# Performance work log

Measured on AMD Instinct MI355X. Metric: run time of the kernel, lower is better.

## Reference

```python
import jax, jax.numpy as jnp
import numpy as np

N = 50000      # nodes
E = 800000     # edges (avg degree 16)
IN = 256       # input feature dim
HID = 128      # hidden dim
H = 4          # heads
C = HID // H   # per-head dim = 32
L = 3          # layers


def setup_inputs() -> dict:
    key = jax.random.key(0)
    ks = jax.random.split(key, 16)
    s = 0.02
    f32 = jnp.float32
    inp = {
        "x": jax.random.normal(ks[0], (N, IN), f32),
        "edge_index": jax.random.randint(ks[1], (2, E), 0, N, dtype=jnp.int32),
        "edge_attr": jax.random.normal(ks[2], (E, 1), f32),
        "Wi": jax.random.normal(ks[3], (IN, HID), f32) * s,
        "bi": jnp.zeros((HID,), f32),
        "Wq": jax.random.normal(ks[4], (L, HID, HID), f32) * s,
        "bq": jnp.zeros((L, HID), f32),
        "Wk": jax.random.normal(ks[5], (L, HID, HID), f32) * s,
        "bk": jnp.zeros((L, HID), f32),
        "Wv": jax.random.normal(ks[6], (L, HID, HID), f32) * s,
        "bv": jnp.zeros((L, HID), f32),
        "We": jax.random.normal(ks[7], (L, 1, HID), f32) * s,      # lin_edge, no bias
        "Wskip": jax.random.normal(ks[8], (L, HID, HID), f32) * s,
        "bskip": jnp.zeros((L, HID), f32),
        "Wbeta": jax.random.normal(ks[9], (L, 3 * HID, 1), f32) * s,  # lin_beta, no bias
        "ln_g": jnp.ones((L, HID), f32),
        "ln_b": jnp.zeros((L, HID), f32),
    }
    return inp


def _layer_norm(x, g, b, eps=1e-5):
    mu = jnp.mean(x, axis=-1, keepdims=True)
    var = jnp.var(x, axis=-1, keepdims=True)
    return (x - mu) * jax.lax.rsqrt(var + eps) * g + b


def _transformer_conv(h, src, dst, edge_attr, Wq, bq, Wk, bk, Wv, bv, We, Wskip, bskip, Wbeta):
    # node-level projections [N, HID]
    q = h @ Wq + bq
    k = h @ Wk + bk
    v = h @ Wv + bv
    e = edge_attr @ We                       # [E, HID] edge embedding
    # per-edge gathered features [E, H, C]
    qi = q[dst].reshape(E, H, C)
    kj = (k[src] + e).reshape(E, H, C)
    vj = (v[src] + e).reshape(E, H, C)
    # attention logits [E, H]
    alpha = jnp.sum(qi * kj, axis=-1) / np.sqrt(C)
    # segment softmax over destination node
    amax = jax.ops.segment_max(alpha, dst, num_segments=N)   # [N, H]
    ex = jnp.exp(alpha - amax[dst])
    denom = jax.ops.segment_sum(ex, dst, num_segments=N)     # [N, H]
    attn = ex / (denom[dst] + 1e-16)                         # [E, H]
    # scatter-add aggregation -> [N, H, C] -> concat heads [N, HID]
    out = jax.ops.segment_sum(attn[..., None] * vj, dst, num_segments=N).reshape(N, HID)
    # gated skip (beta=True, root_weight=True)
    x_r = h @ Wskip + bskip
    beta = jax.nn.sigmoid(jnp.concatenate([out, x_r, out - x_r], axis=-1) @ Wbeta)  # [N, 1]
    return beta * x_r + (1.0 - beta) * out


def reference(x, edge_index, edge_attr, Wi, bi, Wq, bq, Wk, bk, Wv, bv, We, Wskip, bskip, Wbeta, ln_g, ln_b):
    src = edge_index[0]
    dst = edge_index[1]
    h = x @ Wi + bi
    for l in range(L):
        res = h
        h = _transformer_conv(h, src, dst, edge_attr,
                              Wq[l], bq[l], Wk[l], bk[l], Wv[l], bv[l],
                              We[l], Wskip[l], bskip[l], Wbeta[l])
        h = jax.nn.gelu(h, approximate=False)
        h = _layer_norm(h + res, ln_g[l], ln_b[l])
        # dropout: eval mode -> identity
    return h
```

## Files before the change

### kernel.cpp

```cpp
#include <hip/hip_runtime.h>
#include <math.h>

#define NNODES 50000
#define NEDGES 800000
#define DIN 256
#define DHID 128
#define GBLK 391

typedef __attribute__((ext_vector_type(8))) short short8;
typedef __attribute__((ext_vector_type(4))) float f32x4;
typedef __attribute__((ext_vector_type(2))) float f32x2;

__device__ __forceinline__ unsigned short f2bf(float f) {
    unsigned u = __builtin_bit_cast(unsigned, f);
    u += 0x7fffu + ((u >> 16) & 1u);
    return (unsigned short)(u >> 16);
}
__device__ __forceinline__ float bf2f(unsigned short s) {
    return __builtin_bit_cast(float, (unsigned)s << 16);
}
__device__ __forceinline__ unsigned packbf(float a, float b) {
    return (unsigned)f2bf(a) | ((unsigned)f2bf(b) << 16);
}
__device__ __forceinline__ float dpp_xor1(float x) {
    return __builtin_bit_cast(float, __builtin_amdgcn_update_dpp(0, __builtin_bit_cast(int, x), 0xB1, 0xF, 0xF, true));
}
__device__ __forceinline__ float dpp_xor2(float x) {
    return __builtin_bit_cast(float, __builtin_amdgcn_update_dpp(0, __builtin_bit_cast(int, x), 0x4E, 0xF, 0xF, true));
}
__device__ __forceinline__ float dpp_hmirror(float x) {
    return __builtin_bit_cast(float, __builtin_amdgcn_update_dpp(0, __builtin_bit_cast(int, x), 0x141, 0xF, 0xF, true));
}
__device__ __forceinline__ float dpp_mirror(float x) {
    return __builtin_bit_cast(float, __builtin_amdgcn_update_dpp(0, __builtin_bit_cast(int, x), 0x140, 0xF, 0xF, true));
}
__device__ __forceinline__ float red16(float x) {
    x += dpp_xor1(x);
    x += dpp_xor2(x);
    x += dpp_hmirror(x);
    x += dpp_mirror(x);
    return x;
}

__global__ __launch_bounds__(256) void prep_hist(const float* __restrict__ Wi, const float* __restrict__ Wq,
                                                 const float* __restrict__ Wk, const float* __restrict__ Wv,
                                                 const float* __restrict__ Ws, unsigned short* __restrict__ Wit,
                                                 unsigned short* __restrict__ Wt3, const int* __restrict__ dst,
                                                 int* __restrict__ counts, int pb) {
    if ((int)blockIdx.x < pb) {
        int idx = blockIdx.x * 256 + threadIdx.x;
        if (idx < DHID * DIN) {
            int n = idx >> 8, kk = idx & 255;
            Wit[idx] = f2bf(Wi[kk * DHID + n]);
        }
        int idx2 = idx - DHID * DIN;
        if (idx2 >= 0 && idx2 < 3 * 512 * DHID) {
            int l = idx2 / (512 * DHID);
            int rem = idx2 - l * 512 * DHID;
            int r = rem >> 7;
            int kk = rem & 127;
            int sel = r >> 7, rl = r & 127;
            const float* srcm = sel == 0 ? Wq : sel == 1 ? Wk : sel == 2 ? Wv : Ws;
            Wt3[idx2] = f2bf(srcm[l * DHID * DHID + kk * DHID + rl]);
        }
    } else {
        int e = (blockIdx.x - pb) * 256 + threadIdx.x;
        if (e < NEDGES) atomicAdd(&counts[dst[e]], 1);
    }
}

__global__ __launch_bounds__(256) void k_scan_block(const int* __restrict__ in, int* __restrict__ out,
                                                    int* __restrict__ partials, int n) {
    __shared__ int sh[256];
    int tid = threadIdx.x;
    int i = blockIdx.x * 256 + tid;
    int vv = (i < n) ? in[i] : 0;
    sh[tid] = vv;
    __syncthreads();
    for (int off = 1; off < 256; off <<= 1) {
        int t = (tid >= off) ? sh[tid - off] : 0;
        __syncthreads();
        sh[tid] += t;
        __syncthreads();
    }
    if (i < n) out[i] = sh[tid];
    if (tid == 255) partials[blockIdx.x] = sh[255];
}

__global__ __launch_bounds__(256) void k_apply2(const int* __restrict__ partials, int* __restrict__ row_ptr, int n,
                                                int nb) {
    __shared__ int sh[256];
    int tid = threadIdx.x;
    int vv = (tid < nb) ? partials[tid] : 0;
    sh[tid] = vv;
    __syncthreads();
    for (int off = 1; off < 256; off <<= 1) {
        int t = (tid >= off) ? sh[tid - off] : 0;
        __syncthreads();
        sh[tid] += t;
        __syncthreads();
    }
    int i = blockIdx.x * 256 + tid;
    if (i < n) {
        int add = blockIdx.x ? sh[blockIdx.x - 1] : 0;
        row_ptr[i + 1] += add;
    }
    if (i == 0) row_ptr[0] = 0;
}

__global__ __launch_bounds__(256) void scatter_gemm(const float* __restrict__ A, const unsigned short* __restrict__ Wt,
                                                    const float* __restrict__ bias, unsigned* __restrict__ h32, int M,
                                                    const int* __restrict__ src, const int* __restrict__ dst,
                                                    const float* __restrict__ ea, const int* __restrict__ row_ptr,
                                                    int* __restrict__ fill, unsigned* __restrict__ esrc) {
    __shared__ short As[128 * 128];
    const int tid = threadIdx.x;
    if ((int)blockIdx.x >= GBLK) {
        int e = (blockIdx.x - GBLK) * 256 + tid;
        if (e < NEDGES) {
            int d = dst[e];
            int old = atomicSub(&fill[d], 1);
            int pos = row_ptr[d] + old - 1;
            unsigned pk = (unsigned)src[e] | ((unsigned)f2bf(ea[e]) << 16);
            __builtin_nontemporal_store(pk, &esrc[pos]);
        }
        return;
    }
    const int lane = tid & 63;
    const int wid = tid >> 6;
    const int row0 = blockIdx.x * 128;
    const int wr = (wid & 1) * 64;
    const int wc = (wid >> 1) * 64;
    f32x4 acc[4][4] = {};
    const int srow = tid >> 1;
    const int sk = (tid & 1) * 64;
    const int grow = min(row0 + srow, M - 1);
    for (int kt = 0; kt < 2; ++kt) {
        const float* ap = A + (size_t)grow * DIN + kt * 128 + sk;
#pragma unroll
        for (int i = 0; i < 8; ++i) {
            float4 f0 = *(const float4*)(ap + i * 8);
            float4 f1 = *(const float4*)(ap + i * 8 + 4);
            short8 s;
            s[0] = f2bf(f0.x); s[1] = f2bf(f0.y); s[2] = f2bf(f0.z); s[3] = f2bf(f0.w);
            s[4] = f2bf(f1.x); s[5] = f2bf(f1.y); s[6] = f2bf(f1.z); s[7] = f2bf(f1.w);
            int g = (sk >> 3) + i;
            *(short8*)(&As[srow * 128 + ((g ^ (srow & 7)) << 3)]) = s;
        }
        __syncthreads();
#pragma unroll
        for (int ks = 0; ks < 4; ++ks) {
            short8 a[4], b[4];
#pragma unroll
            for (int m = 0; m < 4; ++m) {
                int r = wr + m * 16 + (lane & 15);
                int g = ks * 4 + (lane >> 4);
                a[m] = *(const short8*)(&As[r * 128 + ((g ^ (r & 7)) << 3)]);
            }
#pragma unroll
            for (int n = 0; n < 4; ++n) {
                int c = wc + n * 16 + (lane & 15);
                b[n] = *(const short8*)(Wt + (size_t)c * DIN + kt * 128 + ks * 32 + (lane >> 4) * 8);
            }
#pragma unroll
            for (int m = 0; m < 4; ++m)
#pragma unroll
                for (int n = 0; n < 4; ++n)
                    acc[m][n] = __builtin_amdgcn_mfma_f32_16x16x32_bf16(a[m], b[n], acc[m][n], 0, 0, 0);
        }
        __syncthreads();
    }
    float* my = ((float*)As) + wid * 1024;
    float bb[4];
#pragma unroll
    for (int n = 0; n < 4; ++n) bb[n] = bias[wc + n * 16 + (lane & 15)];
    const int rr = lane >> 2;
    const int cb = lane & 3;
#pragma unroll
    for (int m = 0; m < 4; ++m) {
#pragma unroll
        for (int n = 0; n < 4; ++n) {
            int lc = n * 16 + (lane & 15);
#pragma unroll
            for (int j = 0; j < 4; ++j) {
                int row = (lane >> 4) * 4 + j;
                my[row * 64 + (((lc >> 2) ^ (row & 7)) << 2) + (lc & 3)] = acc[m][n][j] + bb[n];
            }
        }
        float vals[16];
#pragma unroll
        for (int s = 0; s < 4; ++s) {
            int gx = (cb * 4 + s) ^ (rr & 7);
            f32x4 t4 = *(const f32x4*)(my + rr * 64 + gx * 4);
            vals[s * 4 + 0] = t4.x; vals[s * 4 + 1] = t4.y; vals[s * 4 + 2] = t4.z; vals[s * 4 + 3] = t4.w;
        }
        int grow2 = row0 + wr + m * 16 + rr;
        if (grow2 < M) {
            unsigned pk[8];
#pragma unroll
            for (int d = 0; d < 8; ++d) pk[d] = packbf(vals[2 * d], vals[2 * d + 1]);
            unsigned* op = h32 + (size_t)grow2 * 64 + (wc >> 1) + cb * 8;
            *(uint4*)op = make_uint4(pk[0], pk[1], pk[2], pk[3]);
            *(uint4*)(op + 4) = make_uint4(pk[4], pk[5], pk[6], pk[7]);
        }
    }
}

__global__ __launch_bounds__(512) void gemm_qkvs(const unsigned short* __restrict__ A,
                                                 const unsigned short* __restrict__ Wt, const float* __restrict__ bq,
                                                 const float* __restrict__ bk, const float* __restrict__ bv,
                                                 const float* __restrict__ bs, unsigned* __restrict__ q32,
                                                 unsigned* __restrict__ kv, unsigned* __restrict__ xr32, int M) {
    __shared__ short As[128 * 128];
    const int tid = threadIdx.x;
    const int lane = tid & 63;
    const int wid = tid >> 6;
    const int row0 = blockIdx.x * 128;
    const int sel = wid >> 2;
    const int wr = (wid & 1) * 64;
    const int wc = ((wid >> 1) & 1) * 64;
    f32x4 acc0[4][4] = {}, acc1[4][4] = {};
    {
        const int srow = tid >> 2;
        const int sk = (tid & 3) * 32;
        const int grow = min(row0 + srow, M - 1);
        const unsigned short* ap = A + (size_t)grow * DHID + sk;
#pragma unroll
        for (int i = 0; i < 4; ++i) {
            short8 s = *(const short8*)(ap + i * 8);
            int g = (sk >> 3) + i;
            *(short8*)(&As[srow * 128 + ((g ^ (srow & 7)) << 3)]) = s;
        }
    }
    __syncthreads();
    const int b0base = sel ? 128 : 0;
    const int b1base = sel ? 256 : 384;
#pragma unroll
    for (int ks = 0; ks < 4; ++ks) {
        short8 a[4], b0[4], b1[4];
#pragma unroll
        for (int m = 0; m < 4; ++m) {
            int r = wr + m * 16 + (lane & 15);
            int g = ks * 4 + (lane >> 4);
            a[m] = *(const short8*)(&As[r * 128 + ((g ^ (r & 7)) << 3)]);
        }
#pragma unroll
        for (int n = 0; n < 4; ++n) {
            int rb = wc + n * 16 + (lane & 15);
            b0[n] = *(const short8*)(Wt + (size_t)(b0base + rb) * DHID + ks * 32 + (lane >> 4) * 8);
            b1[n] = *(const short8*)(Wt + (size_t)(b1base + rb) * DHID + ks * 32 + (lane >> 4) * 8);
        }
#pragma unroll
        for (int m = 0; m < 4; ++m)
#pragma unroll
            for (int n = 0; n < 4; ++n) {
                acc0[m][n] = __builtin_amdgcn_mfma_f32_16x16x32_bf16(a[m], b0[n], acc0[m][n], 0, 0, 0);
                acc1[m][n] = __builtin_amdgcn_mfma_f32_16x16x32_bf16(a[m], b1[n], acc1[m][n], 0, 0, 0);
            }
    }
    __syncthreads();
    float* my = ((float*)As) + wid * 1024;
    const float* bias0 = sel ? bk : bq;
    const float* bias1 = sel ? bv : bs;
    float bb0[4], bb1[4];
#pragma unroll
    for (int n = 0; n < 4; ++n) {
        int c = wc + n * 16 + (lane & 15);
        bb0[n] = bias0[c];
        bb1[n] = bias1[c];
    }
    const int rr = lane >> 2;
    const int cb = lane & 3;
#pragma unroll
    for (int m = 0; m < 4; ++m) {
        float vals0[16], vals1[16];
#pragma unroll
        for (int n = 0; n < 4; ++n) {
            int lc = n * 16 + (lane & 15);
#pragma unroll
            for (int j = 0; j < 4; ++j) {
                int row = (lane >> 4) * 4 + j;
                my[row * 64 + (((lc >> 2) ^ (row & 7)) << 2) + (lc & 3)] = acc0[m][n][j] + bb0[n];
            }
        }
#pragma unroll
        for (int s = 0; s < 4; ++s) {
            int gx = (cb * 4 + s) ^ (rr & 7);
            f32x4 t4 = *(const f32x4*)(my + rr * 64 + gx * 4);
            vals0[s * 4 + 0] = t4.x; vals0[s * 4 + 1] = t4.y; vals0[s * 4 + 2] = t4.z; vals0[s * 4 + 3] = t4.w;
        }
#pragma unroll
        for (int n = 0; n < 4; ++n) {
            int lc = n * 16 + (lane & 15);
#pragma unroll
            for (int j = 0; j < 4; ++j) {
                int row = (lane >> 4) * 4 + j;
                my[row * 64 + (((lc >> 2) ^ (row & 7)) << 2) + (lc & 3)] = acc1[m][n][j] + bb1[n];
            }
        }
#pragma unroll
        for (int s = 0; s < 4; ++s) {
            int gx = (cb * 4 + s) ^ (rr & 7);
            f32x4 t4 = *(const f32x4*)(my + rr * 64 + gx * 4);
            vals1[s * 4 + 0] = t4.x; vals1[s * 4 + 1] = t4.y; vals1[s * 4 + 2] = t4.z; vals1[s * 4 + 3] = t4.w;
        }
        int grow2 = row0 + wr + m * 16 + rr;
        if (grow2 < M) {
            size_t obase = (size_t)grow2 * 64 + (wc >> 1) + cb * 8;
            if (sel == 0) {
                unsigned p0[8], p1[8];
#pragma unroll
                for (int d = 0; d < 8; ++d) {
                    p0[d] = packbf(vals0[2 * d], vals0[2 * d + 1]);
                    p1[d] = packbf(vals1[2 * d], vals1[2 * d + 1]);
                }
                *(uint4*)(q32 + obase) = make_uint4(p0[0], p0[1], p0[2], p0[3]);
                *(uint4*)(q32 + obase + 4) = make_uint4(p0[4], p0[5], p0[6], p0[7]);
                *(uint4*)(xr32 + obase) = make_uint4(p1[0], p1[1], p1[2], p1[3]);
                *(uint4*)(xr32 + obase + 4) = make_uint4(p1[4], p1[5], p1[6], p1[7]);
            } else {
                unsigned pk[8];
#pragma unroll
                for (int d = 0; d < 8; ++d) {
                    unsigned u = (unsigned)__builtin_amdgcn_cvt_pk_fp8_f32(vals0[2 * d], vals0[2 * d + 1], 0, false);
                    u = (unsigned)__builtin_amdgcn_cvt_pk_fp8_f32(vals1[2 * d], vals1[2 * d + 1], (int)u, true);
                    pk[d] = u;
                }
                *(uint4*)(kv + obase) = make_uint4(pk[0], pk[1], pk[2], pk[3]);
                *(uint4*)(kv + obase + 4) = make_uint4(pk[4], pk[5], pk[6], pk[7]);
            }
        }
    }
}

__global__ __launch_bounds__(256) void node_attn_fuse(const unsigned* __restrict__ q32,
                                                      const unsigned* __restrict__ kv, const unsigned* __restrict__ esrc,
                                                      const float* __restrict__ We, const int* __restrict__ row_ptr,
                                                      const unsigned* __restrict__ xr32, const unsigned* res32,
                                                      const float* __restrict__ Wb, const float* __restrict__ lng,
                                                      const float* __restrict__ lnb, unsigned* houtb, float* houtf) {
    const int tid = threadIdx.x;
    const int lane = tid & 63;
    const int lnl = lane & 15;
    const int gbase = lane & 48;
    const int node = blockIdx.x * 16 + (tid >> 4);
    const int base = row_ptr[node], end = row_ptr[node + 1];
    const float SC = 0.25505654047688565f;
    const float THR = 8.0f;

    float qv[8], wev[8];
    {
        uint4 qw = *(const uint4*)(q32 + (size_t)node * 64 + 4 * lnl);
        unsigned qd[4] = {qw.x, qw.y, qw.z, qw.w};
#pragma unroll
        for (int t = 0; t < 4; ++t) {
            qv[2 * t] = bf2f((unsigned short)qd[t]) * SC;
            qv[2 * t + 1] = bf2f((unsigned short)(qd[t] >> 16)) * SC;
        }
        float4 wlo = *(const float4*)(We + 8 * lnl);
        float4 whi = *(const float4*)(We + 8 * lnl + 4);
        wev[0] = wlo.x; wev[1] = wlo.y; wev[2] = wlo.z; wev[3] = wlo.w;
        wev[4] = whi.x; wev[5] = whi.y; wev[6] = whi.z; wev[7] = whi.w;
    }
    float qwe;
    {
        float s = 0.f;
#pragma unroll
        for (int i = 0; i < 8; ++i) s = fmaf(qv[i], wev[i], s);
        s += dpp_xor1(s);
        s += dpp_xor2(s);
        qwe = s;
    }

    float m = -1e30f, sden = 0.f, tacc = 0.f;
    float acc[8] = {};
    const unsigned* kvp = kv + 4 * lnl;

    for (int off = 0; ; off += 16) {
        int cnt = min(end - base - off, 16);
        if (__all(cnt <= 0)) break;
        unsigned u_l = 0;
        if (lnl < cnt) u_l = esrc[base + off + lnl];
        int cm = max(cnt, 0);
        cm = max(cm, __shfl_xor(cm, 16));
        cm = max(cm, __shfl_xor(cm, 32));
        unsigned ue_n = __shfl((int)u_l, gbase);
        uint4 kw_n = *(const uint4*)(kvp + (size_t)(ue_n & 0xFFFFu) * 64);
        for (int j = 0; j < cm; ++j) {
            uint4 kw = kw_n;
            float av = bf2f((unsigned short)(ue_n >> 16));
            bool valid = j < cnt;
            if (j + 1 < cm) {
                ue_n = __shfl((int)u_l, gbase + j + 1);
                kw_n = *(const uint4*)(kvp + (size_t)(ue_n & 0xFFFFu) * 64);
            }
            unsigned kd[4] = {kw.x, kw.y, kw.z, kw.w};
            float vj[8];
            float p = 0.f;
#pragma unroll
            for (int t = 0; t < 4; ++t) {
                f32x2 kk = __builtin_amdgcn_cvt_pk_f32_fp8((int)kd[t], false);
                f32x2 vv = __builtin_amdgcn_cvt_pk_f32_fp8((int)kd[t], true);
                p = fmaf(qv[2 * t], kk.x, p);
                p = fmaf(qv[2 * t + 1], kk.y, p);
                vj[2 * t] = vv.x;
                vj[2 * t + 1] = vv.y;
            }
            p += dpp_xor1(p);
            p += dpp_xor2(p);
            p = fmaf(av, qwe, p);
            p = valid ? p : -3e38f;
            if (__any(p - m > THR)) {
                float mn2 = fmaxf(m, p);
                float wgt = exp2f(p - mn2);
                float sc = exp2f(m - mn2);
                sden = fmaf(sden, sc, wgt);
                tacc = fmaf(tacc, sc, wgt * av);
#pragma unroll
                for (int i = 0; i < 8; ++i) acc[i] = fmaf(acc[i], sc, wgt * vj[i]);
                m = mn2;
            } else {
                float wgt = exp2f(p - m);
                sden += wgt;
                tacc = fmaf(wgt, av, tacc);
#pragma unroll
                for (int i = 0; i < 8; ++i) acc[i] = fmaf(wgt, vj[i], acc[i]);
            }
        }
    }

    float rden = 1.f / (sden + 1e-16f);
    float o[8];
#pragma unroll
    for (int i = 0; i < 8; ++i) o[i] = fmaf(tacc, wev[i], acc[i]) * rden;

    float x[8];
    {
        uint4 xw = *(const uint4*)(xr32 + (size_t)node * 64 + 4 * lnl);
        unsigned xd[4] = {xw.x, xw.y, xw.z, xw.w};
#pragma unroll
        for (int t = 0; t < 4; ++t) {
            x[2 * t] = bf2f((unsigned short)xd[t]);
            x[2 * t + 1] = bf2f((unsigned short)(xd[t] >> 16));
        }
    }
    float bl = 0.f;
#pragma unroll
    for (int t = 0; t < 2; ++t) {
        float4 w0 = *(const float4*)(Wb + 8 * lnl + 4 * t);
        float4 w1 = *(const float4*)(Wb + 128 + 8 * lnl + 4 * t);
        float4 w2 = *(const float4*)(Wb + 256 + 8 * lnl + 4 * t);
        bl = fmaf(o[4 * t], w0.x, bl); bl = fmaf(o[4 * t + 1], w0.y, bl);
        bl = fmaf(o[4 * t + 2], w0.z, bl); bl = fmaf(o[4 * t + 3], w0.w, bl);
        bl = fmaf(x[4 * t], w1.x, bl); bl = fmaf(x[4 * t + 1], w1.y, bl);
        bl = fmaf(x[4 * t + 2], w1.z, bl); bl = fmaf(x[4 * t + 3], w1.w, bl);
        bl = fmaf(o[4 * t] - x[4 * t], w2.x, bl); bl = fmaf(o[4 * t + 1] - x[4 * t + 1], w2.y, bl);
        bl = fmaf(o[4 * t + 2] - x[4 * t + 2], w2.z, bl); bl = fmaf(o[4 * t + 3] - x[4 * t + 3], w2.w, bl);
    }
    bl = red16(bl);
    float beta = 1.f / (1.f + __expf(-bl));
    float tpre[8];
    {
        uint4 rw = *(const uint4*)(res32 + (size_t)node * 64 + 4 * lnl);
        unsigned rd[4] = {rw.x, rw.y, rw.z, rw.w};
#pragma unroll
        for (int i = 0; i < 8; ++i) {
            float gg = beta * x[i] + (1.f - beta) * o[i];
            gg = 0.5f * gg * (1.f + erff(gg * 0.70710678118654752f));
            float rv = (i & 1) ? bf2f((unsigned short)(rd[i >> 1] >> 16)) : bf2f((unsigned short)rd[i >> 1]);
            tpre[i] = gg + rv;
        }
    }
    float su = 0.f, sq = 0.f;
#pragma unroll
    for (int i = 0; i < 8; ++i) {
        su += tpre[i];
        sq = fmaf(tpre[i], tpre[i], sq);
    }
    su = red16(su);
    sq = red16(sq);
    float mu = su * (1.f / 128.f);
    float var = sq * (1.f / 128.f) - mu * mu;
    float inv = rsqrtf(var + 1e-5f);
    float4 g0 = *(const float4*)(lng + 8 * lnl);
    float4 g1 = *(const float4*)(lng + 8 * lnl + 4);
    float4 b0 = *(const float4*)(lnb + 8 * lnl);
    float4 b1 = *(const float4*)(lnb + 8 * lnl + 4);
    float gg[8] = {g0.x, g0.y, g0.z, g0.w, g1.x, g1.y, g1.z, g1.w};
    float bb[8] = {b0.x, b0.y, b0.z, b0.w, b1.x, b1.y, b1.z, b1.w};
    float ov[8];
#pragma unroll
    for (int i = 0; i < 8; ++i) ov[i] = (tpre[i] - mu) * inv * gg[i] + bb[i];
    if (houtf) {
        float* op = houtf + (size_t)node * 128 + 8 * lnl;
        *(float4*)op = make_float4(ov[0], ov[1], ov[2], ov[3]);
        *(float4*)(op + 4) = make_float4(ov[4], ov[5], ov[6], ov[7]);
    } else {
        unsigned pk[4];
#pragma unroll
        for (int d = 0; d < 4; ++d) pk[d] = packbf(ov[2 * d], ov[2 * d + 1]);
        *(uint4*)(houtb + (size_t)node * 64 + 4 * lnl) = make_uint4(pk[0], pk[1], pk[2], pk[3]);
    }
}

extern "C" void kernel_launch(void* const* d_in, const int* in_sizes, int n_in, void* d_out, int out_size,
                              void* d_ws, size_t ws_size, hipStream_t stream) {
    const float* x = (const float*)d_in[0];
    const int* ei = (const int*)d_in[1];
    const float* ea = (const float*)d_in[2];
    const float* Wi = (const float*)d_in[3];
    const float* bi = (const float*)d_in[4];
    const float* Wq = (const float*)d_in[5];
    const float* bq = (const float*)d_in[6];
    const float* Wk = (const float*)d_in[7];
    const float* bk = (const float*)d_in[8];
    const float* Wv = (const float*)d_in[9];
    const float* bv = (const float*)d_in[10];
    const float* We = (const float*)d_in[11];
    const float* Wskip = (const float*)d_in[12];
    const float* bskip = (const float*)d_in[13];
    const float* Wbeta = (const float*)d_in[14];
    const float* lng = (const float*)d_in[15];
    const float* lnb = (const float*)d_in[16];

    const int* srcp = ei;
    const int* dstp = ei + NEDGES;

    char* p = (char*)d_ws;
    auto alloc = [&](size_t bytes) {
        void* r = (void*)p;
        p += (bytes + 255) & ~(size_t)255;
        return r;
    };
    unsigned* h32 = (unsigned*)alloc((size_t)NNODES * 64 * 4);
    unsigned* q32 = (unsigned*)alloc((size_t)NNODES * 64 * 4);
    unsigned* xr32 = (unsigned*)alloc((size_t)NNODES * 64 * 4);
    unsigned* kv = (unsigned*)alloc((size_t)NNODES * 64 * 4);
    unsigned short* Wit = (unsigned short*)alloc((size_t)DHID * DIN * 2);
    unsigned short* Wt3 = (unsigned short*)alloc((size_t)3 * 512 * DHID * 2);
    int* counts = (int*)alloc((size_t)NNODES * 4);
    int* row_ptr = (int*)alloc((size_t)(NNODES + 1) * 4);
    unsigned* esrc = (unsigned*)alloc((size_t)NEDGES * 4);
    int* partials = (int*)alloc(256 * 4);

    const int EB = (NEDGES + 255) / 256;
    const int NB = (NNODES + 255) / 256;
    const int WB = NNODES / 16;
    const int PB = (DHID * DIN + 3 * 512 * DHID + 255) / 256;

    hipMemsetAsync(counts, 0, (size_t)NNODES * 4, stream);
    prep_hist<<<PB + EB, 256, 0, stream>>>(Wi, Wq, Wk, Wv, Wskip, Wit, Wt3, dstp, counts, PB);
    k_scan_block<<<NB, 256, 0, stream>>>(counts, row_ptr + 1, partials, NNODES);
    k_apply2<<<NB, 256, 0, stream>>>(partials, row_ptr, NNODES, NB);
    scatter_gemm<<<GBLK + EB, 256, 0, stream>>>(x, Wit, bi, h32, NNODES, srcp, dstp, ea, row_ptr, counts, esrc);

    for (int l = 0; l < 3; ++l) {
        const size_t bo = (size_t)l * 128;
        gemm_qkvs<<<GBLK, 512, 0, stream>>>((const unsigned short*)h32, Wt3 + (size_t)l * 512 * DHID, bq + bo, bk + bo,
                                            bv + bo, bskip + bo, q32, kv, xr32, NNODES);
        node_attn_fuse<<<WB, 256, 0, stream>>>(q32, kv, esrc, We + bo, row_ptr, xr32, h32,
                                               Wbeta + (size_t)l * 384, lng + bo, lnb + bo, h32,
                                               (l == 2) ? (float*)d_out : nullptr);
    }
}
```

Measured before the change: 325.8 us.

## Replace atomic CSR scatter with two-pass bucketed edge sort and unroll attention loop

```diff
diff --git a/kernel.cpp b/kernel.cpp
--- a/kernel.cpp
+++ b/kernel.cpp
@@ -6,6 +6,8 @@
 #define DIN 256
 #define DHID 128
 #define GBLK 391
+#define NBUCK 196
+#define CHUNK 4096
 
 typedef __attribute__((ext_vector_type(8))) short short8;
 typedef __attribute__((ext_vector_type(4))) float f32x4;
@@ -108,24 +110,81 @@
     if (i == 0) row_ptr[0] = 0;
 }
 
-__global__ __launch_bounds__(256) void scatter_gemm(const float* __restrict__ A, const unsigned short* __restrict__ Wt,
-                                                    const float* __restrict__ bias, unsigned* __restrict__ h32, int M,
-                                                    const int* __restrict__ src, const int* __restrict__ dst,
-                                                    const float* __restrict__ ea, const int* __restrict__ row_ptr,
-                                                    int* __restrict__ fill, unsigned* __restrict__ esrc) {
+__global__ __launch_bounds__(256) void bin_edges(const int* __restrict__ src, const int* __restrict__ dst,
+                                                 const float* __restrict__ ea, const int* __restrict__ row_ptr,
+                                                 int* __restrict__ bfill, unsigned* __restrict__ brec,
+                                                 unsigned char* __restrict__ bdst) {
+    __shared__ int hist[NBUCK];
+    __shared__ int lbase[NBUCK];
+    __shared__ int gbase[NBUCK];
+    __shared__ int cnt[NBUCK];
+    __shared__ unsigned rec4[CHUNK];
+    __shared__ unsigned char dl8[CHUNK];
+    __shared__ unsigned char bk8[CHUNK];
+    const int tid = threadIdx.x;
+    const int e0 = blockIdx.x * CHUNK;
+    const int n = min(NEDGES - e0, CHUNK);
+    for (int i = tid; i < NBUCK; i += 256) hist[i] = 0;
+    __syncthreads();
+    for (int i = tid; i < n; i += 256) atomicAdd(&hist[dst[e0 + i] >> 8], 1);
+    __syncthreads();
+    if (tid == 0) {
+        int run = 0;
+        for (int b = 0; b < NBUCK; ++b) {
+            lbase[b] = run;
+            run += hist[b];
+        }
+    }
+    __syncthreads();
+    for (int b = tid; b < NBUCK; b += 256) {
+        int h = hist[b];
+        int off = h ? atomicAdd(&bfill[b], h) : 0;
+        gbase[b] = row_ptr[b << 8] + off;
+        cnt[b] = lbase[b];
+    }
+    __syncthreads();
+    for (int i = tid; i < n; i += 256) {
+        int d = dst[e0 + i];
+        int b = d >> 8;
+        int lp = atomicAdd(&cnt[b], 1);
+        rec4[lp] = (unsigned)src[e0 + i] | ((unsigned)f2bf(ea[e0 + i]) << 16);
+        dl8[lp] = (unsigned char)(d & 255);
+        bk8[lp] = (unsigned char)b;
+    }
+    __syncthreads();
+    for (int i = tid; i < n; i += 256) {
+        int b = bk8[i];
+        int pos = gbase[b] + (i - lbase[b]);
+        brec[pos] = rec4[i];
+        bdst[pos] = dl8[i];
+    }
+}
+
+__global__ __launch_bounds__(256) void sort_bucket(const unsigned* __restrict__ brec,
+                                                   const unsigned char* __restrict__ bdst,
+                                                   const int* __restrict__ row_ptr, unsigned* __restrict__ esrc) {
+    __shared__ int rp[257];
+    __shared__ int cnt[256];
+    const int b = blockIdx.x;
+    const int d0 = b << 8;
+    const int nmax = min(256, NNODES - d0);
+    const int tid = threadIdx.x;
+    for (int i = tid; i <= nmax; i += 256) rp[i] = row_ptr[d0 + i];
+    cnt[tid] = 0;
+    __syncthreads();
+    const int base = rp[0], end = rp[nmax];
+    for (int i = base + tid; i < end; i += 256) {
+        unsigned rec = brec[i];
+        int d = bdst[i];
+        int rank = atomicAdd(&cnt[d], 1);
+        esrc[rp[d] + rank] = rec;
+    }
+}
+
+__global__ __launch_bounds__(256) void gemm_in(const float* __restrict__ A, const unsigned short* __restrict__ Wt,
+                                               const float* __restrict__ bias, unsigned* __restrict__ h32, int M) {
     __shared__ short As[128 * 128];
     const int tid = threadIdx.x;
-    if ((int)blockIdx.x >= GBLK) {
-        int e = (blockIdx.x - GBLK) * 256 + tid;
-        if (e < NEDGES) {
-            int d = dst[e];
-            int old = atomicSub(&fill[d], 1);
-            int pos = row_ptr[d] + old - 1;
-            unsigned pk = (unsigned)src[e] | ((unsigned)f2bf(ea[e]) << 16);
-            __builtin_nontemporal_store(pk, &esrc[pos]);
-        }
-        return;
-    }
     const int lane = tid & 63;
     const int wid = tid >> 6;
     const int row0 = blockIdx.x * 128;
@@ -384,47 +443,62 @@
         int cm = max(cnt, 0);
         cm = max(cm, __shfl_xor(cm, 16));
         cm = max(cm, __shfl_xor(cm, 32));
-        unsigned ue_n = __shfl((int)u_l, gbase);
-        uint4 kw_n = *(const uint4*)(kvp + (size_t)(ue_n & 0xFFFFu) * 64);
-        for (int j = 0; j < cm; ++j) {
-            uint4 kw = kw_n;
-            float av = bf2f((unsigned short)(ue_n >> 16));
-            bool valid = j < cnt;
-            if (j + 1 < cm) {
-                ue_n = __shfl((int)u_l, gbase + j + 1);
-                kw_n = *(const uint4*)(kvp + (size_t)(ue_n & 0xFFFFu) * 64);
-            }
-            unsigned kd[4] = {kw.x, kw.y, kw.z, kw.w};
-            float vj[8];
-            float p = 0.f;
+        unsigned ue0 = (unsigned)__shfl((int)u_l, gbase + 0);
+        unsigned ue1 = (unsigned)__shfl((int)u_l, gbase + 1);
+        uint4 kw0 = *(const uint4*)(kvp + (size_t)(ue0 & 0xFFFFu) * 64);
+        uint4 kw1 = *(const uint4*)(kvp + (size_t)(ue1 & 0xFFFFu) * 64);
+        for (int j = 0; j < cm; j += 2) {
+            uint4 ka = kw0, kb = kw1;
+            unsigned ua = ue0, ub = ue1;
+            if (j + 2 < cm) {
+                ue0 = (unsigned)__shfl((int)u_l, gbase + j + 2);
+                ue1 = (unsigned)__shfl((int)u_l, gbase + j + 3);
+                kw0 = *(const uint4*)(kvp + (size_t)(ue0 & 0xFFFFu) * 64);
+                kw1 = *(const uint4*)(kvp + (size_t)(ue1 & 0xFFFFu) * 64);
+            }
+            float av0 = bf2f((unsigned short)(ua >> 16));
+            float av1 = bf2f((unsigned short)(ub >> 16));
+            unsigned kd0[4] = {ka.x, ka.y, ka.z, ka.w};
+            unsigned kd1[4] = {kb.x, kb.y, kb.z, kb.w};
+            float vj0[8], vj1[8];
+            float p0 = 0.f, p1 = 0.f;
 #pragma unroll
             for (int t = 0; t < 4; ++t) {
-                f32x2 kk = __builtin_amdgcn_cvt_pk_f32_fp8((int)kd[t], false);
-                f32x2 vv = __builtin_amdgcn_cvt_pk_f32_fp8((int)kd[t], true);
-                p = fmaf(qv[2 * t], kk.x, p);
-                p = fmaf(qv[2 * t + 1], kk.y, p);
-                vj[2 * t] = vv.x;
-                vj[2 * t + 1] = vv.y;
-            }
-            p += dpp_xor1(p);
-            p += dpp_xor2(p);
-            p = fmaf(av, qwe, p);
-            p = valid ? p : -3e38f;
-            if (__any(p - m > THR)) {
-                float mn2 = fmaxf(m, p);
-                float wgt = exp2f(p - mn2);
+                f32x2 k0 = __builtin_amdgcn_cvt_pk_f32_fp8((int)kd0[t], false);
+                f32x2 v0 = __builtin_amdgcn_cvt_pk_f32_fp8((int)kd0[t], true);
+                f32x2 k1 = __builtin_amdgcn_cvt_pk_f32_fp8((int)kd1[t], false);
+                f32x2 v1 = __builtin_amdgcn_cvt_pk_f32_fp8((int)kd1[t], true);
+                p0 = fmaf(qv[2 * t], k0.x, p0);
+                p0 = fmaf(qv[2 * t + 1], k0.y, p0);
+                p1 = fmaf(qv[2 * t], k1.x, p1);
+                p1 = fmaf(qv[2 * t + 1], k1.y, p1);
+                vj0[2 * t] = v0.x; vj0[2 * t + 1] = v0.y;
+                vj1[2 * t] = v1.x; vj1[2 * t + 1] = v1.y;
+            }
+            p0 += dpp_xor1(p0);
+            p0 += dpp_xor2(p0);
+            p1 += dpp_xor1(p1);
+            p1 += dpp_xor2(p1);
+            p0 = fmaf(av0, qwe, p0);
+            p1 = fmaf(av1, qwe, p1);
+            p0 = (j < cnt) ? p0 : -3e38f;
+            p1 = (j + 1 < cnt) ? p1 : -3e38f;
+            float pm = fmaxf(p0, p1);
+            if (__any(pm - m > THR)) {
+                float mn2 = fmaxf(m, pm);
                 float sc = exp2f(m - mn2);
-                sden = fmaf(sden, sc, wgt);
-                tacc = fmaf(tacc, sc, wgt * av);
-#pragma unroll
-                for (int i = 0; i < 8; ++i) acc[i] = fmaf(acc[i], sc, wgt * vj[i]);
+                float w0 = exp2f(p0 - mn2), w1 = exp2f(p1 - mn2);
+                sden = fmaf(sden, sc, w0 + w1);
+                tacc = fmaf(tacc, sc, fmaf(w0, av0, w1 * av1));
+#pragma unroll
+                for (int i = 0; i < 8; ++i) acc[i] = fmaf(acc[i], sc, fmaf(w0, vj0[i], w1 * vj1[i]));
                 m = mn2;
             } else {
-                float wgt = exp2f(p - m);
-                sden += wgt;
-                tacc = fmaf(wgt, av, tacc);
-#pragma unroll
-                for (int i = 0; i < 8; ++i) acc[i] = fmaf(wgt, vj[i], acc[i]);
+                float w0 = exp2f(p0 - m), w1 = exp2f(p1 - m);
+                sden += w0 + w1;
+                tacc = fmaf(w0, av0, fmaf(w1, av1, tacc));
+#pragma unroll
+                for (int i = 0; i < 8; ++i) acc[i] = fmaf(w0, vj0[i], fmaf(w1, vj1[i], acc[i]));
             }
         }
     }
@@ -538,21 +612,27 @@
     unsigned* kv = (unsigned*)alloc((size_t)NNODES * 64 * 4);
     unsigned short* Wit = (unsigned short*)alloc((size_t)DHID * DIN * 2);
     unsigned short* Wt3 = (unsigned short*)alloc((size_t)3 * 512 * DHID * 2);
-    int* counts = (int*)alloc((size_t)NNODES * 4);
+    int* counts = (int*)alloc((size_t)(NNODES + 256) * 4);
+    int* bfill = counts + NNODES;
     int* row_ptr = (int*)alloc((size_t)(NNODES + 1) * 4);
     unsigned* esrc = (unsigned*)alloc((size_t)NEDGES * 4);
+    unsigned* brec = (unsigned*)alloc((size_t)NEDGES * 4);
+    unsigned char* bdst = (unsigned char*)alloc((size_t)NEDGES);
     int* partials = (int*)alloc(256 * 4);
 
     const int EB = (NEDGES + 255) / 256;
     const int NB = (NNODES + 255) / 256;
     const int WB = NNODES / 16;
     const int PB = (DHID * DIN + 3 * 512 * DHID + 255) / 256;
-
-    hipMemsetAsync(counts, 0, (size_t)NNODES * 4, stream);
+    const int AB = (NEDGES + CHUNK - 1) / CHUNK;
+
+    hipMemsetAsync(counts, 0, (size_t)(NNODES + 256) * 4, stream);
     prep_hist<<<PB + EB, 256, 0, stream>>>(Wi, Wq, Wk, Wv, Wskip, Wit, Wt3, dstp, counts, PB);
+    gemm_in<<<GBLK, 256, 0, stream>>>(x, Wit, bi, h32, NNODES);
     k_scan_block<<<NB, 256, 0, stream>>>(counts, row_ptr + 1, partials, NNODES);
     k_apply2<<<NB, 256, 0, stream>>>(partials, row_ptr, NNODES, NB);
-    scatter_gemm<<<GBLK + EB, 256, 0, stream>>>(x, Wit, bi, h32, NNODES, srcp, dstp, ea, row_ptr, counts, esrc);
+    bin_edges<<<AB, 256, 0, stream>>>(srcp, dstp, ea, row_ptr, bfill, brec, bdst);
+    sort_bucket<<<NBUCK, 256, 0, stream>>>(brec, bdst, row_ptr, esrc);
 
     for (int l = 0; l < 3; ++l) {
         const size_t bo = (size_t)l * 128;
```

New measurement: 312.7 us. -4.0%, faster.
